# Optimization experiments

Measured on AMD Instinct MI355X. Metric: run time of the kernel, lower is better.

Reference implementation:

```python
import jax, jax.numpy as jnp
import numpy as np

N_HEAD = 16


def setup_inputs() -> dict:
    key = jax.random.key(0)
    ks = jax.random.split(key, 5)
    B, T, C = 4, 4096, 2048
    H = N_HEAD
    x = jax.random.normal(ks[0], (B, T, C), dtype=jnp.float32)
    # torch Linear weights are (out_features, in_features); bias=False
    Wa = jax.random.normal(ks[1], (C, C), dtype=jnp.float32) * 0.02
    Wp = jax.random.normal(ks[2], (C, C), dtype=jnp.float32) * 0.02
    temp = jnp.ones((H, 1), dtype=jnp.float32)
    denom_bias = jnp.zeros((H, T, 1), dtype=jnp.float32)  # block_size == T
    return {"x": x, "Wa": Wa, "Wp": Wp, "temp": temp, "denom_bias": denom_bias}


def reference(x, Wa, Wp, temp, denom_bias):
    B, T, C = x.shape
    H = N_HEAD
    D = C // H
    # c_attn (no bias): y = x @ Wa^T
    w = jnp.einsum('btc,oc->bto', x, Wa)
    w = w.reshape(B, T, H, D).transpose(0, 2, 1, 3)  # (B,H,T,D)
    w_sq = w * w
    # running second-moment denominator along time
    denom = jnp.maximum(jnp.cumsum(w_sq, axis=2), 1e-12)
    w_normed = w_sq / denom + denom_bias[:, :T, :]          # (B,H,T,D)
    tmp = jnp.sum(w_normed, axis=-1) * temp                 # (B,H,T), temp (H,1) broadcasts
    Pi = jax.nn.softmax(tmp, axis=1)                        # softmax over heads
    # token-statistics attention: running Pi-weighted mean of w_sq
    dots = jnp.cumsum(w_sq * Pi[..., None], axis=2) / (jnp.cumsum(Pi, axis=-1) + 1e-8)[..., None]
    attn = 1.0 / (1.0 + dots)                               # (B,H,T,D)
    y = -(w * Pi[..., None]) * attn                         # (B,H,T,D)
    y = y.transpose(0, 2, 1, 3).reshape(B, T, C)
    # c_proj (no bias)
    y = jnp.einsum('btc,oc->bto', y, Wp)
    return y
```

## Files before the change

kernel.cpp:

```cpp
#include <hip/hip_runtime.h>
#include <hip/hip_bf16.h>
#include <stdint.h>

#define BB 4
#define TT 4096
#define CC 2048
#define HH 16
#define DD 128
#define MM (BB*TT)
#define KK CC
#define NNx CC
#define NTP 16

#define NCH 128
#define CHL (TT/NCH)

typedef unsigned short u16;
typedef unsigned int   u32;
typedef __bf16 bf16x8 __attribute__((ext_vector_type(8)));
typedef float  f32x4  __attribute__((ext_vector_type(4)));

__device__ __forceinline__ float bf2f(u32 lo) {
  union { u32 u; float f; } z; z.u = lo << 16; return z.f;
}
__device__ __forceinline__ u16 f2bf(float f) {
  union { float f; u32 u; } z; z.f = f;
  u32 u = z.u;
  return (u16)((u + 0x7FFFu + ((u >> 16) & 1u)) >> 16);
}
__device__ __forceinline__ void unpack8(uint4 v, float* a) {
  a[0]=bf2f(v.x&0xffffu); a[1]=bf2f(v.x>>16);
  a[2]=bf2f(v.y&0xffffu); a[3]=bf2f(v.y>>16);
  a[4]=bf2f(v.z&0xffffu); a[5]=bf2f(v.z>>16);
  a[6]=bf2f(v.w&0xffffu); a[7]=bf2f(v.w>>16);
}

__global__ void cvt_f32_bf16(const float* __restrict__ in, u16* __restrict__ out, long n) {
  long i = ((long)blockIdx.x * blockDim.x + threadIdx.x) * 8;
  if (i >= n) return;
  float4 v0 = *(const float4*)(in + i);
  float4 v1 = *(const float4*)(in + i + 4);
  uint4 o;
  o.x = (u32)f2bf(v0.x) | ((u32)f2bf(v0.y) << 16);
  o.y = (u32)f2bf(v0.z) | ((u32)f2bf(v0.w) << 16);
  o.z = (u32)f2bf(v1.x) | ((u32)f2bf(v1.y) << 16);
  o.w = (u32)f2bf(v1.z) | ((u32)f2bf(v1.w) << 16);
  *(uint4*)(out + i) = o;
}

__device__ __forceinline__ void gload16(const void* g, void* l) {
  __builtin_amdgcn_global_load_lds(
      (__attribute__((address_space(1))) void*)g,
      (__attribute__((address_space(3))) void*)l, 16, 0, 0);
}

template<int OUTF32, int EPI>
__global__ __launch_bounds__(512, 2)
void gemm256(const u16* __restrict__ A, const u16* __restrict__ Bm,
             float* __restrict__ Cf, u16* __restrict__ Cb,
             float* __restrict__ S1)
{
  __shared__ u16 As[4][8192];
  __shared__ u16 Bs[4][8192];
  const int tid  = threadIdx.x;
  const int wid  = tid >> 6;
  const int lane = tid & 63;
  const int wm = wid >> 2, wn = wid & 3;
  const int fr = lane & 15, kg = lane >> 4;
  const int orig = blockIdx.x;
  const int nid  = ((orig & 7) << 6) | (orig >> 3);
  const int m0 = (nid >> 3) * 256;
  const int n0 = (nid & 7) * 256;

  const int srow = tid >> 2;
  const int sc   = (tid & 3) ^ ((srow >> 1) & 3);
  const u16* gA0 = A  + (size_t)(m0 + srow) * KK + sc * 8;
  const u16* gA1 = gA0 + (size_t)128 * KK;
  const u16* gB0 = Bm + (size_t)(n0 + srow) * KK + sc * 8;
  const u16* gB1 = gB0 + (size_t)128 * KK;
  const int ldst0 = wid * 512;
  const int ldst1 = 4096 + wid * 512;

  const int cs    = kg ^ ((fr >> 1) & 3);
  const int abase = (wm * 128 + fr) * 32 + cs * 8;
  const int bbase = (wn * 64  + fr) * 32 + cs * 8;

  f32x4 acc[8][4];
  #pragma unroll
  for (int i = 0; i < 8; ++i)
    #pragma unroll
    for (int j = 0; j < 4; ++j) acc[i][j] = (f32x4){0.f,0.f,0.f,0.f};

  auto stA = [&](int slot, int ko) {
    gload16(gA0 + ko, &As[slot][ldst0]);
    gload16(gA1 + ko, &As[slot][ldst1]);
  };
  auto stB = [&](int slot, int ko) {
    gload16(gB0 + ko, &Bs[slot][ldst0]);
    gload16(gB1 + ko, &Bs[slot][ldst1]);
  };

  stA(0, 0);  stB(0, 0);
  stA(1, 32); stB(1, 32);
  stA(2, 64); stB(2, 64);
  asm volatile("s_waitcnt vmcnt(8)" ::: "memory");
  __builtin_amdgcn_s_barrier();

  bf16x8 av[4], bv[4];

#define PH(CSLOT, MH, LOADB, STMT, DOWAIT) do {                               \
    _Pragma("unroll")                                                         \
    for (int f = 0; f < 4; ++f)                                               \
      av[f] = *(const bf16x8*)&As[CSLOT][abase + ((MH)*64 + f*16)*32];        \
    if (LOADB) {                                                              \
      _Pragma("unroll")                                                       \
      for (int f = 0; f < 4; ++f)                                             \
        bv[f] = *(const bf16x8*)&Bs[CSLOT][bbase + f*16*32];                  \
    }                                                                         \
    STMT;                                                                     \
    if (DOWAIT) asm volatile("s_waitcnt vmcnt(8)" ::: "memory");              \
    __builtin_amdgcn_s_barrier();                                             \
    __builtin_amdgcn_s_setprio(1);                                            \
    _Pragma("unroll")                                                         \
    for (int f = 0; f < 4; ++f)                                               \
      _Pragma("unroll")                                                       \
      for (int n = 0; n < 4; ++n)                                             \
        acc[(MH)*4+f][n] = __builtin_amdgcn_mfma_f32_16x16x32_bf16(          \
            av[f], bv[n], acc[(MH)*4+f][n], 0, 0, 0);                         \
    __builtin_amdgcn_s_setprio(0);                                            \
    __builtin_amdgcn_s_barrier();                                             \
  } while (0)

  for (int it = 0; it < NTP; ++it) {
    const int kb = it * 128;
    const bool nx = (it + 1 < NTP);
    PH(0, 0, 1, stA(3, kb + 96), 0);
    PH(0, 1, 0, stB(3, kb + 96), 1);
    PH(1, 0, 1, if (nx) stA(0, kb + 128), 0);
    PH(1, 1, 0, if (nx) stB(0, kb + 128), 1);
    PH(2, 0, 1, if (nx) stA(1, kb + 160), 0);
    PH(2, 1, 0, if (nx) stB(1, kb + 160), 1);
    PH(3, 0, 1, if (nx) stA(2, kb + 192), 0);
    PH(3, 1, 0, if (nx) stB(2, kb + 192), 1);
  }
#undef PH

  const int row0 = m0 + wm * 128 + kg * 4;
  const int col0 = n0 + wn * 64 + fr;
  if (OUTF32) {
    #pragma unroll
    for (int mf = 0; mf < 8; ++mf)
      #pragma unroll
      for (int nf = 0; nf < 4; ++nf)
        #pragma unroll
        for (int r = 0; r < 4; ++r)
          Cf[(size_t)(row0 + mf*16 + r) * NNx + col0 + nf*16] = acc[mf][nf][r];
  } else {
    float csum[4][4];
    #pragma unroll
    for (int p = 0; p < 4; ++p)
      #pragma unroll
      for (int nf = 0; nf < 4; ++nf) csum[p][nf] = 0.f;
    #pragma unroll
    for (int mf = 0; mf < 8; ++mf)
      #pragma unroll
      for (int nf = 0; nf < 4; ++nf)
        #pragma unroll
        for (int r = 0; r < 4; ++r) {
          u16 hb = f2bf(acc[mf][nf][r]);
          Cb[(size_t)(row0 + mf*16 + r) * NNx + col0 + nf*16] = hb;
          if (EPI) { float av_ = bf2f(hb); csum[mf>>1][nf] += av_ * av_; }
        }
    if (EPI) {
      const int b   = m0 >> 12;
      const int ch0 = ((m0 & (TT-1)) >> 5) + wm * 4;
      #pragma unroll
      for (int p = 0; p < 4; ++p)
        #pragma unroll
        for (int nf = 0; nf < 4; ++nf) {
          float v = csum[p][nf];
          v += __shfl_xor(v, 16, 64);
          v += __shfl_xor(v, 32, 64);
          if (kg == 0)
            S1[(size_t)(ch0 + p) * (BB*CC) + b * CC + col0 + nf*16] = v;
        }
    }
  }
}

__global__ void excl_big(float* __restrict__ p) {
  const int g = blockIdx.x * 256 + threadIdx.x;
  float run = 0.f;
  for (int ch = 0; ch < NCH; ++ch) {
    float v = p[(size_t)ch * (BB*CC) + g];
    p[(size_t)ch * (BB*CC) + g] = run;
    run += v;
  }
}
__global__ void excl_sp(float* __restrict__ p) {
  const int g = threadIdx.x;
  float run = 0.f;
  for (int ch = 0; ch < NCH; ++ch) {
    float v = p[ch * (BB*HH) + g];
    p[ch * (BB*HH) + g] = run;
    run += v;
  }
}

__global__ __launch_bounds__(256)
void pass_c(const u16* __restrict__ w, float* __restrict__ S,
            float* __restrict__ SP, float* __restrict__ Pi,
            const float* __restrict__ temp, const float* __restrict__ dbias)
{
  __shared__ float sm[2][HH];
  const int ch = blockIdx.x, b = blockIdx.y;
  const int tid = threadIdx.x;
  const int h = tid >> 4;
  const int t0 = ch * CHL;
  const u16* wrow = w + ((size_t)b*TT + t0) * CC + tid*8;
  float* Srow = S + (size_t)ch * (BB*CC) + b * CC + tid*8;
  float c0[8], s2[8];
  #pragma unroll
  for (int j = 0; j < 8; ++j) { c0[j] = Srow[j]; s2[j] = 0.f; }
  const float th = temp[h];
  const float* db = dbias + (size_t)h * TT + t0;
  float sp = 0.f;
  uint4 v = *(const uint4*)wrow;
  for (int t = 0; t < CHL; ++t) {
    uint4 vn = v;
    if (t + 1 < CHL) vn = *(const uint4*)(wrow + (size_t)(t+1) * CC);
    float a2[8];
    { float a[8]; unpack8(v, a);
      #pragma unroll
      for (int j = 0; j < 8; ++j) a2[j] = a[j]*a[j]; }
    float val = 0.f;
    #pragma unroll
    for (int j = 0; j < 8; ++j) {
      c0[j] += a2[j];
      val += a2[j] * __builtin_amdgcn_rcpf(fmaxf(c0[j], 1e-12f));
    }
    val += __shfl_xor(val, 1, 64);
    val += __shfl_xor(val, 2, 64);
    val += __shfl_xor(val, 4, 64);
    val += __shfl_xor(val, 8, 64);
    const float tmp = th * (val + (float)DD * db[t]);
    if ((tid & 15) == 0) sm[t & 1][h] = tmp;
    __syncthreads();
    float m = -1e30f;
    #pragma unroll
    for (int hh = 0; hh < HH; ++hh) m = fmaxf(m, sm[t & 1][hh]);
    float ssum = 0.f;
    #pragma unroll
    for (int hh = 0; hh < HH; ++hh) ssum += __expf(sm[t & 1][hh] - m);
    const float pi = __expf(sm[t & 1][h] - m) * __builtin_amdgcn_rcpf(ssum);
    sp += pi;
    #pragma unroll
    for (int j = 0; j < 8; ++j) s2[j] += a2[j] * pi;
    if ((tid & 15) == 0) Pi[((size_t)b*TT + t0 + t) * HH + h] = pi;
    v = vn;
  }
  #pragma unroll
  for (int j = 0; j < 8; ++j) Srow[j] = s2[j];
  if ((tid & 15) == 0) SP[ch * (BB*HH) + b * HH + h] = sp;
}

__global__ __launch_bounds__(256)
void pass_d(const u16* __restrict__ w, const float* __restrict__ S2,
            const float* __restrict__ SP, const float* __restrict__ Pi,
            u16* __restrict__ ymid)
{
  const int ch = blockIdx.x, b = blockIdx.y;
  const int tid = threadIdx.x;
  const int h = tid >> 4;
  const int t0 = ch * CHL;
  const u16* wrow = w + ((size_t)b*TT + t0) * CC + tid*8;
  u16* yrow = ymid + ((size_t)b*TT + t0) * CC + tid*8;
  const float* Srow = S2 + (size_t)ch * (BB*CC) + b * CC + tid*8;
  float c2[8];
  #pragma unroll
  for (int j = 0; j < 8; ++j) c2[j] = Srow[j];
  float cp = SP[ch * (BB*HH) + b * HH + h];
  const float* prow = Pi + ((size_t)b*TT + t0) * HH + h;
  uint4 v = *(const uint4*)wrow;
  for (int t = 0; t < CHL; ++t) {
    uint4 vn = v;
    if (t + 1 < CHL) vn = *(const uint4*)(wrow + (size_t)(t+1) * CC);
    const float pi = prow[(size_t)t * HH];
    cp += pi;
    const float invp = __builtin_amdgcn_rcpf(cp + 1e-8f);
    float a[8]; unpack8(v, a);
    float y[8];
    #pragma unroll
    for (int j = 0; j < 8; ++j) {
      const float a2 = a[j]*a[j];
      c2[j] += a2 * pi;
      const float d = c2[j] * invp;
      y[j] = -(a[j] * pi) * __builtin_amdgcn_rcpf(1.f + d);
    }
    uint4 o;
    o.x = (u32)f2bf(y[0]) | ((u32)f2bf(y[1]) << 16);
    o.y = (u32)f2bf(y[2]) | ((u32)f2bf(y[3]) << 16);
    o.z = (u32)f2bf(y[4]) | ((u32)f2bf(y[5]) << 16);
    o.w = (u32)f2bf(y[6]) | ((u32)f2bf(y[7]) << 16);
    *(uint4*)(yrow + (size_t)t * CC) = o;
    v = vn;
  }
}

extern "C" void kernel_launch(void* const* d_in, const int* in_sizes, int n_in,
                              void* d_out, int out_size, void* d_ws, size_t ws_size,
                              hipStream_t stream) {
  const float* x     = (const float*)d_in[0];
  const float* Wa    = (const float*)d_in[1];
  const float* Wp    = (const float*)d_in[2];
  const float* temp  = (const float*)d_in[3];
  const float* dbias = (const float*)d_in[4];
  float* out = (float*)d_out;

  char* ws = (char*)d_ws;
  u16*  xb   = (u16*)(ws);
  u16*  Wab  = (u16*)(ws + 67108864);
  u16*  Wpb  = (u16*)(ws + 75497472);
  u16*  wbuf = (u16*)(ws + 83886080);
  float* S1  = (float*)(ws + 150994944);
  float* SP  = (float*)(ws + 155189248);
  float* Pi  = (float*)(ws + 67108864);
  u16*  ymid = xb;

  cvt_f32_bf16<<<(MM*(long)KK)/8/256, 256, 0, stream>>>(x,  xb,  (long)MM*KK);
  cvt_f32_bf16<<<((long)CC*CC)/8/256, 256, 0, stream>>>(Wa, Wab, (long)CC*CC);
  cvt_f32_bf16<<<((long)CC*CC)/8/256, 256, 0, stream>>>(Wp, Wpb, (long)CC*CC);

  gemm256<0,1><<<512, 512, 0, stream>>>(xb, Wab, nullptr, wbuf, S1);

  excl_big<<<(BB*CC)/256, 256, 0, stream>>>(S1);

  dim3 gc(NCH, BB);
  pass_c<<<gc, 256, 0, stream>>>(wbuf, S1, SP, Pi, temp, dbias);

  excl_big<<<(BB*CC)/256, 256, 0, stream>>>(S1);
  excl_sp<<<1, 64, 0, stream>>>(SP);

  pass_d<<<gc, 256, 0, stream>>>(wbuf, S1, SP, Pi, ymid);

  gemm256<1,0><<<512, 512, 0, stream>>>(ymid, Wpb, out, nullptr, nullptr);
}
```

Measured before the change: 385.7 us.

## Fuse conversion launches, parallelize chunk scans per wave, drop GEMM prefetch guards

Merges the three fp32-to-bf16 conversion launches into one kernel that picks its source buffer by index. Replaces the serial per-column exclusive scans over 128 chunks with a wave-parallel shuffle scan, one wavefront per column. In the GEMM pipeline, the conditional prefetch on the last iteration becomes an unconditional load clamped to offset 0, which removes the branch but issues redundant loads at the tail. The scan kernels were latency-bound serial loops, so the wave version mainly cuts their dependency chain, at the cost of more launched threads.

```diff
diff --git a/kernel.cpp b/kernel.cpp
--- a/kernel.cpp
+++ b/kernel.cpp
@@ -35,17 +35,24 @@
   a[6]=bf2f(v.w&0xffffu); a[7]=bf2f(v.w>>16);
 }
 
-__global__ void cvt_f32_bf16(const float* __restrict__ in, u16* __restrict__ out, long n) {
+__global__ void cvt3(const float* __restrict__ x, const float* __restrict__ wa,
+                     const float* __restrict__ wp, u16* __restrict__ ox,
+                     u16* __restrict__ oa, u16* __restrict__ op) {
+  const long nx = (long)MM * KK;
+  const long nw = (long)CC * CC;
   long i = ((long)blockIdx.x * blockDim.x + threadIdx.x) * 8;
-  if (i >= n) return;
-  float4 v0 = *(const float4*)(in + i);
-  float4 v1 = *(const float4*)(in + i + 4);
+  const float* in; u16* out; long j;
+  if (i < nx)            { in = x;  out = ox; j = i; }
+  else if (i < nx + nw)  { in = wa; out = oa; j = i - nx; }
+  else                   { in = wp; out = op; j = i - nx - nw; }
+  float4 v0 = *(const float4*)(in + j);
+  float4 v1 = *(const float4*)(in + j + 4);
   uint4 o;
   o.x = (u32)f2bf(v0.x) | ((u32)f2bf(v0.y) << 16);
   o.y = (u32)f2bf(v0.z) | ((u32)f2bf(v0.w) << 16);
   o.z = (u32)f2bf(v1.x) | ((u32)f2bf(v1.y) << 16);
   o.w = (u32)f2bf(v1.z) | ((u32)f2bf(v1.w) << 16);
-  *(uint4*)(out + i) = o;
+  *(uint4*)(out + j) = o;
 }
 
 __device__ __forceinline__ void gload16(const void* g, void* l) {
@@ -92,10 +99,12 @@
     for (int j = 0; j < 4; ++j) acc[i][j] = (f32x4){0.f,0.f,0.f,0.f};
 
   auto stA = [&](int slot, int ko) {
+    ko = (ko < KK) ? ko : 0;
     gload16(gA0 + ko, &As[slot][ldst0]);
     gload16(gA1 + ko, &As[slot][ldst1]);
   };
   auto stB = [&](int slot, int ko) {
+    ko = (ko < KK) ? ko : 0;
     gload16(gB0 + ko, &Bs[slot][ldst0]);
     gload16(gB1 + ko, &Bs[slot][ldst1]);
   };
@@ -133,15 +142,14 @@
 
   for (int it = 0; it < NTP; ++it) {
     const int kb = it * 128;
-    const bool nx = (it + 1 < NTP);
     PH(0, 0, 1, stA(3, kb + 96), 0);
     PH(0, 1, 0, stB(3, kb + 96), 1);
-    PH(1, 0, 1, if (nx) stA(0, kb + 128), 0);
-    PH(1, 1, 0, if (nx) stB(0, kb + 128), 1);
-    PH(2, 0, 1, if (nx) stA(1, kb + 160), 0);
-    PH(2, 1, 0, if (nx) stB(1, kb + 160), 1);
-    PH(3, 0, 1, if (nx) stA(2, kb + 192), 0);
-    PH(3, 1, 0, if (nx) stB(2, kb + 192), 1);
+    PH(1, 0, 1, stA(0, kb + 128), 0);
+    PH(1, 1, 0, stB(0, kb + 128), 1);
+    PH(2, 0, 1, stA(1, kb + 160), 0);
+    PH(2, 1, 0, stB(1, kb + 160), 1);
+    PH(3, 0, 1, stA(2, kb + 192), 0);
+    PH(3, 1, 0, stB(2, kb + 192), 1);
   }
 #undef PH
 
@@ -188,23 +196,24 @@
   }
 }
 
-__global__ void excl_big(float* __restrict__ p) {
-  const int g = blockIdx.x * 256 + threadIdx.x;
-  float run = 0.f;
-  for (int ch = 0; ch < NCH; ++ch) {
-    float v = p[(size_t)ch * (BB*CC) + g];
-    p[(size_t)ch * (BB*CC) + g] = run;
-    run += v;
-  }
-}
-__global__ void excl_sp(float* __restrict__ p) {
-  const int g = threadIdx.x;
-  float run = 0.f;
-  for (int ch = 0; ch < NCH; ++ch) {
-    float v = p[ch * (BB*HH) + g];
-    p[ch * (BB*HH) + g] = run;
-    run += v;
-  }
+template<int S>
+__global__ __launch_bounds__(256)
+void excl_scan_wave(float* __restrict__ p, int ncol) {
+  const int w = (int)((blockIdx.x * 256 + threadIdx.x) >> 6);
+  const int l = threadIdx.x & 63;
+  if (w >= ncol) return;
+  float a = p[(size_t)l * S + w];
+  float b = p[(size_t)(64 + l) * S + w];
+  float ia = a, ib = b;
+  #pragma unroll
+  for (int off = 1; off < 64; off <<= 1) {
+    float ta = __shfl_up(ia, off, 64);
+    float tb = __shfl_up(ib, off, 64);
+    if (l >= off) { ia += ta; ib += tb; }
+  }
+  float totA = __shfl(ia, 63, 64);
+  p[(size_t)l * S + w]        = ia - a;
+  p[(size_t)(64 + l) * S + w] = totA + ib - b;
 }
 
 __global__ __launch_bounds__(256)
@@ -327,19 +336,17 @@
   float* Pi  = (float*)(ws + 67108864);
   u16*  ymid = xb;
 
-  cvt_f32_bf16<<<(MM*(long)KK)/8/256, 256, 0, stream>>>(x,  xb,  (long)MM*KK);
-  cvt_f32_bf16<<<((long)CC*CC)/8/256, 256, 0, stream>>>(Wa, Wab, (long)CC*CC);
-  cvt_f32_bf16<<<((long)CC*CC)/8/256, 256, 0, stream>>>(Wp, Wpb, (long)CC*CC);
+  cvt3<<<20480, 256, 0, stream>>>(x, Wa, Wp, xb, Wab, Wpb);
 
   gemm256<0,1><<<512, 512, 0, stream>>>(xb, Wab, nullptr, wbuf, S1);
 
-  excl_big<<<(BB*CC)/256, 256, 0, stream>>>(S1);
+  excl_scan_wave<BB*CC><<<2048, 256, 0, stream>>>(S1, BB*CC);
 
   dim3 gc(NCH, BB);
   pass_c<<<gc, 256, 0, stream>>>(wbuf, S1, SP, Pi, temp, dbias);
 
-  excl_big<<<(BB*CC)/256, 256, 0, stream>>>(S1);
-  excl_sp<<<1, 64, 0, stream>>>(SP);
+  excl_scan_wave<BB*CC><<<2048, 256, 0, stream>>>(S1, BB*CC);
+  excl_scan_wave<BB*HH><<<16, 256, 0, stream>>>(SP, BB*HH);
 
   pass_d<<<gc, 256, 0, stream>>>(wbuf, S1, SP, Pi, ymid);
 
```

After: 402.5 us. 1.04x slower.
